# Performance work log

Measured on AMD Instinct MI355X. Metric: run time of the kernel, lower is better.

## Reference

```python
import jax, jax.numpy as jnp
import numpy as np

B, L, D, H, HD, K, MAXLEN = 4, 2048, 1024, 16, 64, 32, 2048


def setup_inputs() -> dict:
    key = jax.random.key(0)
    ks = jax.random.split(key, 8)
    s = 0.02  # init scale (stand-in for lecun-normal magnitude)
    return {
        "inputs_q": jax.random.normal(ks[0], (B, L, D), jnp.float32),
        "inputs_kv": jax.random.normal(ks[1], (B, L, D), jnp.float32),
        "Wv": jax.random.normal(ks[2], (D, H, HD), jnp.float32) * s,   # value DenseGeneral kernel
        "bv": jnp.zeros((H, HD), jnp.float32),                          # value bias
        "r1": jax.random.normal(ks[3], (H, MAXLEN, K), jnp.float32) * s,  # param 'random1'
        "r2": jax.random.normal(ks[4], (H, K, MAXLEN), jnp.float32) * s,  # param 'random2'
        "Wo": jax.random.normal(ks[5], (H, HD, D), jnp.float32) * s,   # output DenseGeneral kernel
        "bo": jnp.zeros((D,), jnp.float32),                             # output bias
    }


def reference(inputs_q, inputs_kv, Wv, bv, r1, r2, Wo, bo):
    # SynthesizerAttention with ignore_dot_product=True, mode='factorized_random',
    # no masks, deterministic (no dropout).
    qlen = inputs_q.shape[-2]
    kvlen = inputs_kv.shape[-2]
    # value projection: [B, Lkv, H, HD]; key=value, query=inputs_q (unused for scores)
    v = jnp.einsum('bnd,dhk->bnhk', inputs_kv, Wv) + bv
    # factorized random synthetic scores: [H, Lq, Lkv]
    syn = jnp.einsum('hlk,hkn->hln', r1[:, :qlen, :], r2[:, :, :kvlen])
    # softmax over the key/value axis (norm_dims in synthetic_attention).
    # Scores are batch-independent, so softmax once per head (broadcast over B).
    attn = jax.nn.softmax(syn, axis=-1)
    # weighted sum over values: [B, Lq, H, HD]
    y = jnp.einsum('hln,bnhk->blhk', attn, v)
    # output projection over (H, HD): [B, Lq, D]
    return jnp.einsum('blhk,hkd->bld', y, Wo) + bo
```

## Files before the change

kernel.cpp:

```cpp
#include <hip/hip_runtime.h>
#include <hip/hip_bf16.h>

#define LL 2048

typedef __bf16 bf16x8 __attribute__((ext_vector_type(8)));
typedef __bf16 bf16x4 __attribute__((ext_vector_type(4)));
typedef float f32x4 __attribute__((ext_vector_type(4)));

__device__ inline void gl_lds16(const __bf16* g, __bf16* l) {
    __builtin_amdgcn_global_load_lds((const __attribute__((address_space(1))) void*)g,
                                     (__attribute__((address_space(3))) void*)l, 16, 0, 0);
}

__global__ __launch_bounds__(256) void prep(const float* __restrict__ inputs_kv,
                                            const float* __restrict__ r1,
                                            const float* __restrict__ Wv,
                                            const float* __restrict__ Wo,
                                            const float* __restrict__ r2,
                                            __bf16* __restrict__ A1,
                                            __bf16* __restrict__ r1b,
                                            __bf16* __restrict__ Wvt,
                                            __bf16* __restrict__ Wot,
                                            __bf16* __restrict__ r2t) {
    __shared__ float Ls[32][65];
    int bid = blockIdx.x;
    const int tid = threadIdx.x;
    if (bid < 4608) {
        const float* in = (bid < 4096) ? inputs_kv : r1;
        __bf16* out = (bid < 4096) ? A1 : r1b;
        const int t = ((bid < 4096) ? bid : bid - 4096) * 256 + tid;
        const float4* in4 = (const float4*)in;
        float4 f0 = in4[t * 2], f1 = in4[t * 2 + 1];
        bf16x8 o;
        o[0] = (__bf16)f0.x; o[1] = (__bf16)f0.y; o[2] = (__bf16)f0.z; o[3] = (__bf16)f0.w;
        o[4] = (__bf16)f1.x; o[5] = (__bf16)f1.y; o[6] = (__bf16)f1.z; o[7] = (__bf16)f1.w;
        *(bf16x8*)&out[(size_t)t * 8] = o;
        return;
    }
    bid -= 4608;
    const float* in;
    __bf16* out;
    int R, C, r0, c0;
    if (bid < 512) {
        in = Wv; out = Wvt; R = 1024; C = 1024;
        c0 = (bid & 15) * 64; r0 = (bid >> 4) * 32;
    } else if (bid < 1024) {
        bid -= 512;
        in = Wo; out = Wot; R = 1024; C = 1024;
        c0 = (bid & 15) * 64; r0 = (bid >> 4) * 32;
    } else {
        bid -= 1024;
        const int bz = bid >> 5;
        in = r2 + (size_t)bz * 65536; out = r2t + (size_t)bz * 65536;
        R = 32; C = 2048;
        c0 = (bid & 31) * 64; r0 = 0;
    }
#pragma unroll
    for (int p = 0; p < 2; ++p) {
        int f = tid + 256 * p;
        int row = f >> 4, c4 = (f & 15) << 2;
        float4 v = *(const float4*)&in[(size_t)(r0 + row) * C + c0 + c4];
        Ls[row][c4 + 0] = v.x; Ls[row][c4 + 1] = v.y;
        Ls[row][c4 + 2] = v.z; Ls[row][c4 + 3] = v.w;
    }
    __syncthreads();
    const int orow = tid >> 2, rc = (tid & 3) << 3;
    bf16x8 o;
#pragma unroll
    for (int j = 0; j < 8; ++j) o[j] = (__bf16)Ls[rc + j][orow];
    *(bf16x8*)&out[(size_t)(c0 + orow) * R + r0 + rc] = o;
}

template <int MODE>
__global__ __launch_bounds__(512) void gemm_bt(const __bf16* __restrict__ A,
                                               const __bf16* __restrict__ Bt,
                                               const float* __restrict__ bias,
                                               void* __restrict__ Cout,
                                               int M, int N, int K) {
    __shared__ alignas(16) __bf16 As[2][128 * 64];
    __shared__ alignas(16) __bf16 Bs[2][128 * 64];
    const int tid = threadIdx.x;
    const int lane = tid & 63;
    const int wid = __builtin_amdgcn_readfirstlane(tid >> 6);
    const int f = blockIdx.y * 8 + blockIdx.x;
    const int g = (f & 7) * 64 + (f >> 3);
    const int row0 = (g >> 3) * 128, col0 = (g & 7) * 128;
    const int l15 = lane & 15, quad = lane >> 4;
    const int wr = wid & 1, wc = wid >> 1;

    const int srow = wid * 16 + (lane >> 3);
    const int skoff = (((lane & 7) ^ (lane >> 3)) << 3);
    const __bf16* gaS = A + (size_t)(row0 + srow) * K + skoff;
    const __bf16* gbS = Bt + (size_t)(col0 + srow) * K + skoff;
    const int lbase = (wid * 16) * 64;

    f32x4 acc[4][2];
#pragma unroll
    for (int i = 0; i < 4; ++i)
#pragma unroll
        for (int j = 0; j < 2; ++j) acc[i][j] = (f32x4){0.f, 0.f, 0.f, 0.f};

    const int nt = K >> 6;

#define STAGE(buf, k0)                                                        \
    {                                                                         \
        _Pragma("unroll")                                                     \
        for (int q = 0; q < 2; ++q) {                                         \
            gl_lds16(gaS + (size_t)(q * 8) * K + (k0), As[buf] + lbase + q * 512); \
            gl_lds16(gbS + (size_t)(q * 8) * K + (k0), Bs[buf] + lbase + q * 512); \
        }                                                                     \
    }

    STAGE(0, 0)

    for (int t = 0; t < nt; ++t) {
        __syncthreads();
        if (t + 1 < nt) {
            const int k0 = (t + 1) << 6;
            if ((t & 1) == 0) STAGE(1, k0) else STAGE(0, k0)
        }
        const __bf16* as = As[t & 1];
        const __bf16* bs = Bs[t & 1];
#pragma unroll
        for (int ksub = 0; ksub < 2; ++ksub) {
            bf16x8 af[4], bfv[2];
            const int ch = ((ksub * 4 + quad) ^ (l15 & 7)) * 8;
#pragma unroll
            for (int i = 0; i < 4; ++i) {
                const int r = wr * 64 + i * 16 + l15;
                af[i] = *(const bf16x8*)&as[r * 64 + ch];
            }
#pragma unroll
            for (int j = 0; j < 2; ++j) {
                const int r = wc * 32 + j * 16 + l15;
                bfv[j] = *(const bf16x8*)&bs[r * 64 + ch];
            }
#pragma unroll
            for (int i = 0; i < 4; ++i)
#pragma unroll
                for (int j = 0; j < 2; ++j)
                    acc[i][j] = __builtin_amdgcn_mfma_f32_16x16x32_bf16(af[i], bfv[j], acc[i][j], 0, 0, 0);
        }
    }
#undef STAGE

#pragma unroll
    for (int i = 0; i < 4; ++i) {
        const int rg = row0 + wr * 64 + i * 16 + quad * 4;
#pragma unroll
        for (int j = 0; j < 2; ++j) {
            const int cg = col0 + wc * 32 + j * 16 + l15;
            const float bb = bias[cg];
            if (MODE == 0) {
                const int b = rg >> 11, n = rg & 2047;
                const int h = cg >> 6, hd = cg & 63;
                const int nc = n >> 6, ks = (n >> 5) & 1, qj = (n >> 3) & 3, j0 = n & 7;
                const int jt = hd >> 4, fl = hd & 15;
                __bf16* V3 = (__bf16*)Cout;
                bf16x4 v;
#pragma unroll
                for (int r = 0; r < 4; ++r) v[r] = (__bf16)(acc[i][j][r] + bb);
                *(bf16x4*)&V3[(size_t)(((h * 32 + nc) * 4 + b) * 4096) +
                              (jt * 2 + ks) * 512 + fl * 32 + qj * 8 + j0] = v;
            } else {
                float* Cf = (float*)Cout;
#pragma unroll
                for (int r = 0; r < 4; ++r)
                    Cf[(size_t)(rg + r) * N + cg] = acc[i][j][r] + bb;
            }
        }
    }
}

__global__ __launch_bounds__(512) void attn_pv_v7(const __bf16* __restrict__ r1b,
                                                  const __bf16* __restrict__ r2t,
                                                  const __bf16* __restrict__ V3,
                                                  __bf16* __restrict__ yb) {
    __shared__ alignas(16) __bf16 Ps[2 * 2 * 4 * 1024];
    const int tid = threadIdx.x;
    const int lane = tid & 63;
    const int w = __builtin_amdgcn_readfirstlane(tid >> 6);
    const int b = w & 3, lh = w >> 2;
    const int l15 = lane & 15, quad = lane >> 4;
    const int id = blockIdx.x;
    const int h = id & 15;
    const int l0 = (id >> 4) << 7;

    bf16x8 bf1[4];
#pragma unroll
    for (int i = 0; i < 4; ++i)
        bf1[i] = *(const bf16x8*)&r1b[(size_t)(h * 2048 + l0 + lh * 64 + i * 16 + l15) * 32 + quad * 8];

    const __bf16* r2p = r2t + (size_t)(h * 2048 + b * 16 + l15) * 32 + quad * 8;
    const __bf16* vp = V3 + (size_t)((h * 32) * 4 + b) * 4096 + l15 * 32 + quad * 8;

    bf16x8 r2f = *(const bf16x8*)r2p;
    bf16x8 vpf[4][2];
#pragma unroll
    for (int jt = 0; jt < 4; ++jt)
#pragma unroll
        for (int ks = 0; ks < 2; ++ks)
            vpf[jt][ks] = *(const bf16x8*)(vp + (jt * 2 + ks) * 512);

    bf16x8 ones;
#pragma unroll
    for (int e = 0; e < 8; ++e) ones[e] = (__bf16)1.0f;

    f32x4 acc[4][4];
    f32x4 den[4];
#pragma unroll
    for (int i = 0; i < 4; ++i) {
        den[i] = (f32x4){0.f, 0.f, 0.f, 0.f};
#pragma unroll
        for (int j = 0; j < 4; ++j) acc[i][j] = (f32x4){0.f, 0.f, 0.f, 0.f};
    }
    const f32x4 zero4 = {0.f, 0.f, 0.f, 0.f};

    const int kw = b >> 1;
    const int jg = (b & 1) * 2 + (quad >> 1);
    const int q4 = (quad & 1) * 4;
    const int swz = (l15 >> 1) & 3;

    f32x4 s[4];
#pragma unroll
    for (int i = 0; i < 4; ++i)
        s[i] = __builtin_amdgcn_mfma_f32_16x16x32_bf16(r2f, bf1[i], zero4, 0, 0, 0);
    r2f = *(const bf16x8*)(r2p + 2048);
    {
        __bf16* ps = &Ps[lh * 4096];
#pragma unroll
        for (int i = 0; i < 4; ++i) {
            bf16x4 p4;
#pragma unroll
            for (int r = 0; r < 4; ++r) p4[r] = (__bf16)__expf(s[i][r]);
            *(bf16x4*)&ps[i * 1024 + kw * 512 + l15 * 32 + ((jg ^ swz) << 3) + q4] = p4;
        }
    }

    for (int c = 0; c < 32; ++c) {
        asm volatile("s_waitcnt lgkmcnt(0)" ::: "memory");
        __builtin_amdgcn_s_barrier();
        const __bf16* ps_r = &Ps[((c & 1) * 2 + lh) * 4096];
        bf16x8 pa[4][2];
#pragma unroll
        for (int i = 0; i < 4; ++i)
#pragma unroll
            for (int ks = 0; ks < 2; ++ks)
                pa[i][ks] = *(const bf16x8*)&ps_r[i * 1024 + ks * 512 + l15 * 32 + ((quad ^ swz) << 3)];
#pragma unroll
        for (int i = 0; i < 4; ++i)
            s[i] = __builtin_amdgcn_mfma_f32_16x16x32_bf16(r2f, bf1[i], zero4, 0, 0, 0);
        const int i2 = (c < 30) ? (c + 2) : 31;
        r2f = *(const bf16x8*)(r2p + (size_t)i2 * 2048);
#pragma unroll
        for (int ks = 0; ks < 2; ++ks) {
#pragma unroll
            for (int i = 0; i < 4; ++i) {
#pragma unroll
                for (int jt = 0; jt < 4; ++jt)
                    acc[i][jt] = __builtin_amdgcn_mfma_f32_16x16x32_bf16(pa[i][ks], vpf[jt][ks],
                                                                         acc[i][jt], 0, 0, 0);
                den[i] = __builtin_amdgcn_mfma_f32_16x16x32_bf16(pa[i][ks], ones, den[i], 0, 0, 0);
            }
        }
        __bf16* ps_w = &Ps[(((c + 1) & 1) * 2 + lh) * 4096];
#pragma unroll
        for (int i = 0; i < 4; ++i) {
            bf16x4 p4;
#pragma unroll
            for (int r = 0; r < 4; ++r) p4[r] = (__bf16)__expf(s[i][r]);
            *(bf16x4*)&ps_w[i * 1024 + kw * 512 + l15 * 32 + ((jg ^ swz) << 3) + q4] = p4;
        }
        const int cv = (c < 31) ? 1 : 0;
        vp += cv * 16384;
#pragma unroll
        for (int jt = 0; jt < 4; ++jt)
#pragma unroll
            for (int ks = 0; ks < 2; ++ks)
                vpf[jt][ks] = *(const bf16x8*)(vp + (jt * 2 + ks) * 512);
    }

#pragma unroll
    for (int i = 0; i < 4; ++i) {
#pragma unroll
        for (int r = 0; r < 4; ++r) {
            const float iv = 1.0f / den[i][r];
            const int l = l0 + lh * 64 + i * 16 + quad * 4 + r;
            const size_t rowbase = ((size_t)b * LL + l) * 1024 + h * 64;
#pragma unroll
            for (int jt = 0; jt < 4; ++jt)
                yb[rowbase + jt * 16 + l15] = (__bf16)(acc[i][jt][r] * iv);
        }
    }
}

extern "C" void kernel_launch(void* const* d_in, const int* in_sizes, int n_in,
                              void* d_out, int out_size, void* d_ws, size_t ws_size,
                              hipStream_t stream) {
    const float* inputs_kv = (const float*)d_in[1];
    const float* Wv = (const float*)d_in[2];
    const float* bv = (const float*)d_in[3];
    const float* r1 = (const float*)d_in[4];
    const float* r2 = (const float*)d_in[5];
    const float* Wo = (const float*)d_in[6];
    const float* bo = (const float*)d_in[7];
    float* out = (float*)d_out;

    char* ws = (char*)d_ws;
    const size_t MB = 1024 * 1024;
    __bf16* A1  = (__bf16*)(ws);
    __bf16* Wvt = (__bf16*)(ws + 16 * MB);
    __bf16* Wot = (__bf16*)(ws + 18 * MB);
    __bf16* r1b = (__bf16*)(ws + 20 * MB);
    __bf16* r2t = (__bf16*)(ws + 22 * MB);
    __bf16* V3  = (__bf16*)(ws + 24 * MB);
    __bf16* yb  = (__bf16*)(ws + 40 * MB);

    prep<<<6144, 256, 0, stream>>>(inputs_kv, r1, Wv, Wo, r2, A1, r1b, Wvt, Wot, r2t);
    gemm_bt<0><<<dim3(8, 64), 512, 0, stream>>>(A1, Wvt, bv, V3, 8192, 1024, 1024);
    attn_pv_v7<<<256, 512, 0, stream>>>(r1b, r2t, V3, yb);
    gemm_bt<1><<<dim3(8, 64), 512, 0, stream>>>(yb, Wot, bo, out, 8192, 1024, 1024);
}
```

Before: 198.5 us.

## Fold log2e into r1 for exp2 softmax; retile GEMMs to 128x64 with 256 threads

The r1 conversion in prep now scales by log2(e), so the attention kernel can use exp2f instead of __expf and skip a multiply per score element. Separately, both projection GEMMs move from 128x128 tiles with 8 waves to 128x64 tiles with 4 waves, doubling the grid to 1024 blocks and changing the block-swizzle mapping. The GEMM change is meant to raise block count and occupancy, at the cost of less B-tile reuse per block. The hidden inner-loop indexing must match the new wave layout, which cannot be confirmed from the visible code.

```diff
diff --git a/kernel.cpp b/kernel.cpp
--- a/kernel.cpp
+++ b/kernel.cpp
@@ -28,12 +28,15 @@
     if (bid < 4608) {
         const float* in = (bid < 4096) ? inputs_kv : r1;
         __bf16* out = (bid < 4096) ? A1 : r1b;
+        const float sc = (bid < 4096) ? 1.0f : 1.44269504088896340736f;
         const int t = ((bid < 4096) ? bid : bid - 4096) * 256 + tid;
         const float4* in4 = (const float4*)in;
         float4 f0 = in4[t * 2], f1 = in4[t * 2 + 1];
         bf16x8 o;
-        o[0] = (__bf16)f0.x; o[1] = (__bf16)f0.y; o[2] = (__bf16)f0.z; o[3] = (__bf16)f0.w;
-        o[4] = (__bf16)f1.x; o[5] = (__bf16)f1.y; o[6] = (__bf16)f1.z; o[7] = (__bf16)f1.w;
+        o[0] = (__bf16)(f0.x * sc); o[1] = (__bf16)(f0.y * sc);
+        o[2] = (__bf16)(f0.z * sc); o[3] = (__bf16)(f0.w * sc);
+        o[4] = (__bf16)(f1.x * sc); o[5] = (__bf16)(f1.y * sc);
+        o[6] = (__bf16)(f1.z * sc); o[7] = (__bf16)(f1.w * sc);
         *(bf16x8*)&out[(size_t)t * 8] = o;
         return;
     }
@@ -72,27 +75,27 @@
 }
 
 template <int MODE>
-__global__ __launch_bounds__(512) void gemm_bt(const __bf16* __restrict__ A,
+__global__ __launch_bounds__(256) void gemm_bt(const __bf16* __restrict__ A,
                                                const __bf16* __restrict__ Bt,
                                                const float* __restrict__ bias,
                                                void* __restrict__ Cout,
                                                int M, int N, int K) {
     __shared__ alignas(16) __bf16 As[2][128 * 64];
-    __shared__ alignas(16) __bf16 Bs[2][128 * 64];
+    __shared__ alignas(16) __bf16 Bs[2][64 * 64];
     const int tid = threadIdx.x;
     const int lane = tid & 63;
     const int wid = __builtin_amdgcn_readfirstlane(tid >> 6);
-    const int f = blockIdx.y * 8 + blockIdx.x;
-    const int g = (f & 7) * 64 + (f >> 3);
-    const int row0 = (g >> 3) * 128, col0 = (g & 7) * 128;
+    const int f = blockIdx.y * 16 + blockIdx.x;
+    const int g = (f & 7) * 128 + (f >> 3);
+    const int row0 = (g >> 4) * 128, col0 = (g & 15) * 64;
     const int l15 = lane & 15, quad = lane >> 4;
     const int wr = wid & 1, wc = wid >> 1;
 
-    const int srow = wid * 16 + (lane >> 3);
     const int skoff = (((lane & 7) ^ (lane >> 3)) << 3);
-    const __bf16* gaS = A + (size_t)(row0 + srow) * K + skoff;
-    const __bf16* gbS = Bt + (size_t)(col0 + srow) * K + skoff;
-    const int lbase = (wid * 16) * 64;
+    const __bf16* gaS = A + (size_t)(row0 + wid * 32 + (lane >> 3)) * K + skoff;
+    const __bf16* gbS = Bt + (size_t)(col0 + wid * 16 + (lane >> 3)) * K + skoff;
+    const int lbaseA = wid * 32 * 64;
+    const int lbaseB = wid * 16 * 64;
 
     f32x4 acc[4][2];
 #pragma unroll
@@ -102,13 +105,14 @@
 
     const int nt = K >> 6;
 
-#define STAGE(buf, k0)                                                        \
-    {                                                                         \
-        _Pragma("unroll")                                                     \
-        for (int q = 0; q < 2; ++q) {                                         \
-            gl_lds16(gaS + (size_t)(q * 8) * K + (k0), As[buf] + lbase + q * 512); \
-            gl_lds16(gbS + (size_t)(q * 8) * K + (k0), Bs[buf] + lbase + q * 512); \
-        }                                                                     \
+#define STAGE(buf, k0)                                                            \
+    {                                                                             \
+        _Pragma("unroll")                                                         \
+        for (int q = 0; q < 4; ++q)                                               \
+            gl_lds16(gaS + (size_t)(q * 8) * K + (k0), As[buf] + lbaseA + q * 512); \
+        _Pragma("unroll")                                                         \
+        for (int q = 0; q < 2; ++q)                                               \
+            gl_lds16(gbS + (size_t)(q * 8) * K + (k0), Bs[buf] + lbaseB + q * 512); \
     }
 
     STAGE(0, 0)
@@ -172,10 +176,10 @@
     }
 }
 
-__global__ __launch_bounds__(512) void attn_pv_v7(const __bf16* __restrict__ r1b,
-                                                  const __bf16* __restrict__ r2t,
-                                                  const __bf16* __restrict__ V3,
-                                                  __bf16* __restrict__ yb) {
+__global__ __launch_bounds__(512) void attn_pv_v7e(const __bf16* __restrict__ r1b,
+                                                   const __bf16* __restrict__ r2t,
+                                                   const __bf16* __restrict__ V3,
+                                                   __bf16* __restrict__ yb) {
     __shared__ alignas(16) __bf16 Ps[2 * 2 * 4 * 1024];
     const int tid = threadIdx.x;
     const int lane = tid & 63;
@@ -232,7 +236,7 @@
         for (int i = 0; i < 4; ++i) {
             bf16x4 p4;
 #pragma unroll
-            for (int r = 0; r < 4; ++r) p4[r] = (__bf16)__expf(s[i][r]);
+            for (int r = 0; r < 4; ++r) p4[r] = (__bf16)exp2f(s[i][r]);
             *(bf16x4*)&ps[i * 1024 + kw * 512 + l15 * 32 + ((jg ^ swz) << 3) + q4] = p4;
         }
     }
@@ -268,7 +272,7 @@
         for (int i = 0; i < 4; ++i) {
             bf16x4 p4;
 #pragma unroll
-            for (int r = 0; r < 4; ++r) p4[r] = (__bf16)__expf(s[i][r]);
+            for (int r = 0; r < 4; ++r) p4[r] = (__bf16)exp2f(s[i][r]);
             *(bf16x4*)&ps_w[i * 1024 + kw * 512 + l15 * 32 + ((jg ^ swz) << 3) + q4] = p4;
         }
         const int cv = (c < 31) ? 1 : 0;
@@ -317,7 +321,7 @@
     __bf16* yb  = (__bf16*)(ws + 40 * MB);
 
     prep<<<6144, 256, 0, stream>>>(inputs_kv, r1, Wv, Wo, r2, A1, r1b, Wvt, Wot, r2t);
-    gemm_bt<0><<<dim3(8, 64), 512, 0, stream>>>(A1, Wvt, bv, V3, 8192, 1024, 1024);
-    attn_pv_v7<<<256, 512, 0, stream>>>(r1b, r2t, V3, yb);
-    gemm_bt<1><<<dim3(8, 64), 512, 0, stream>>>(yb, Wot, bo, out, 8192, 1024, 1024);
-}
+    gemm_bt<0><<<dim3(16, 64), 256, 0, stream>>>(A1, Wvt, bv, V3, 8192, 1024, 1024);
+    attn_pv_v7e<<<256, 512, 0, stream>>>(r1b, r2t, V3, yb);
+    gemm_bt<1><<<dim3(16, 64), 256, 0, stream>>>(yb, Wot, bo, out, 8192, 1024, 1024);
+}
```

Result: slower. 222.6 us (+12.2%).
